# Optimization experiments

Measured on AMD Instinct MI355X. Metric: run time of the kernel, lower is better.

## Reference

```python
import jax, jax.numpy as jnp
import numpy as np

N_NODES = 100000
N_EDGES = 3200000
D_FEAT = 512
HIDDEN = 16
N_CLASSES = 7


def _gcn_conv(x, W, b, src, dst, n_nodes):
    """PyG GCNConv (add_self_loops=True, normalize=True):
    out = D^{-1/2} (A + I) D^{-1/2} X W + b, aggregated at target nodes (dst).
    src/dst already include self loops."""
    h = x @ W  # [N, out_dim] -- transform before scatter (small message dim)
    ones = jnp.ones(dst.shape[0], dtype=x.dtype)
    deg = jax.ops.segment_sum(ones, dst, num_segments=n_nodes)  # in-degree incl. self loop
    dinv = jnp.where(deg > 0, jax.lax.rsqrt(deg), 0.0)
    norm = dinv[src] * dinv[dst]  # [E_tot]
    msg = h[src] * norm[:, None]  # gather + scale
    out = jax.ops.segment_sum(msg, dst, num_segments=n_nodes)  # scatter-add
    return out + b


def setup_inputs() -> dict:
    key = jax.random.key(0)
    k1, k2, k3, k4 = jax.random.split(key, 4)
    x = jax.random.normal(k1, (N_NODES, D_FEAT), dtype=jnp.float32)
    edge_index = jax.random.randint(k2, (2, N_EDGES), 0, N_NODES, dtype=jnp.int64)
    # Glorot-ish init for weights
    W1 = jax.random.normal(k3, (D_FEAT, HIDDEN), dtype=jnp.float32) / np.sqrt(D_FEAT)
    b1 = jnp.zeros((HIDDEN,), dtype=jnp.float32)
    W2 = jax.random.normal(k4, (HIDDEN, N_CLASSES), dtype=jnp.float32) / np.sqrt(HIDDEN)
    b2 = jnp.zeros((N_CLASSES,), dtype=jnp.float32)
    return {"x": x, "edge_index": edge_index, "W1": W1, "b1": b1, "W2": W2, "b2": b2}


def reference(x, edge_index, W1, b1, W2, b2):
    n = x.shape[0]
    loop = jnp.arange(n, dtype=edge_index.dtype)
    src = jnp.concatenate([edge_index[0], loop])  # add self loops (fixed shape)
    dst = jnp.concatenate([edge_index[1], loop])
    h = _gcn_conv(x, W1, b1, src, dst, n)
    h = jax.nn.relu(h)
    # F.dropout(training=self.training): identity in eval/inference baseline
    h = _gcn_conv(h, W2, b2, src, dst, n)
    return jax.nn.log_softmax(h, axis=1)
```

## Files before the change

### kernel.cpp

```cpp
#include <hip/hip_runtime.h>

#define NN 100000
#define NE 3200000
#define DF 512
#define HID 16
#define NC 7
#define NBK 782
#define BCAP 6144
#define SC_B 640
#define SEDG 5000
#define GB 391

__global__ void k_zero_i(int* __restrict__ p, int n) {
    int i = blockIdx.x * blockDim.x + threadIdx.x;
    if (i < n) p[i] = 0;
}

struct SMemScat {
    int stage[SEDG];
    int off[NBK + 1];
    int part[256];
    int cur[NBK];
    int gofs[NBK];
};

__global__ __launch_bounds__(256) void k_fused(const float* __restrict__ x,
                                               const float* __restrict__ W1,
                                               const int* __restrict__ src,
                                               const int* __restrict__ dst,
                                               float* __restrict__ h1,
                                               int* __restrict__ bcnt,
                                               int* __restrict__ pk) {
    __shared__ SMemScat u;
    int tid = threadIdx.x;
    if (blockIdx.x < SC_B) {
        int* stage = u.stage;
        int* off   = u.off;
        int* part  = u.part;
        int* cur   = u.cur;
        int* gofs  = u.gofs;
        int e0 = blockIdx.x * SEDG;
        for (int i = tid; i < NBK; i += 256) cur[i] = 0;
        __syncthreads();
        for (int e = e0 + tid; e < e0 + SEDG; e += 256) atomicAdd(&cur[dst[e] >> 7], 1);
        __syncthreads();
        {
            int base = tid * 4;
            int sum = 0;
#pragma unroll
            for (int j = 0; j < 4; ++j) if (base + j < NBK) sum += cur[base + j];
            part[tid] = sum;
            __syncthreads();
            for (int s2 = 1; s2 < 256; s2 <<= 1) {
                int v = (tid >= s2) ? part[tid - s2] : 0;
                __syncthreads();
                part[tid] += v;
                __syncthreads();
            }
            int run = (tid > 0) ? part[tid - 1] : 0;
#pragma unroll
            for (int j = 0; j < 4; ++j) {
                int idx = base + j;
                if (idx < NBK) { off[idx] = run; run += cur[idx]; }
            }
            if (tid == 0) off[NBK] = SEDG;
        }
        __syncthreads();
        for (int i = tid; i < NBK; i += 256) {
            int h = cur[i];
            int g = h ? atomicAdd(&bcnt[i], h) : 0;
            gofs[i] = g - off[i];
            cur[i] = off[i];
        }
        __syncthreads();
        for (int e = e0 + tid; e < e0 + SEDG; e += 256) {
            int d = dst[e];
            int pos = atomicAdd(&cur[d >> 7], 1);
            stage[pos] = src[e] | ((d & 127) << 17);
        }
        __syncthreads();
        for (int i = tid; i < SEDG; i += 256) {
            int lo = 0, hi = NBK;
            while (hi - lo > 1) { int mid = (lo + hi) >> 1; if (off[mid] <= i) lo = mid; else hi = mid; }
            int idx = gofs[lo] + i;
            if (idx < BCAP) pk[(size_t)lo * BCAP + idx] = stage[i];
        }
        return;
    }
    int gwave = (blockIdx.x - SC_B) * 4 + (tid >> 6);
    int lane = tid & 63;
    long row = (long)gwave * 64 + lane;
    long crow = row < NN ? row : NN - 1;
    const float4* xr = (const float4*)(x + crow * DF);
    float acc[16];
#pragma unroll
    for (int c2 = 0; c2 < 16; ++c2) acc[c2] = 0.f;
#pragma unroll 2
    for (int c = 0; c < 128; ++c) {
        float4 xv = xr[c];
#pragma unroll
        for (int j = 0; j < 4; ++j) {
            float xs = (j == 0) ? xv.x : (j == 1) ? xv.y : (j == 2) ? xv.z : xv.w;
            int k = c * 4 + j;
#pragma unroll
            for (int col = 0; col < 16; ++col)
                acc[col] = fmaf(xs, W1[k * HID + col], acc[col]);
        }
    }
    if (row < NN) {
        float* hp = h1 + row * HID;
#pragma unroll
        for (int q = 0; q < 4; ++q) {
            float4 o;
            o.x = acc[q * 4 + 0]; o.y = acc[q * 4 + 1];
            o.z = acc[q * 4 + 2]; o.w = acc[q * 4 + 3];
            *(float4*)(hp + q * 4) = o;
        }
    }
}

__global__ __launch_bounds__(256) void k_sortB(const int* __restrict__ bcnt,
                                               int* __restrict__ pk,
                                               float* __restrict__ dinv,
                                               float* __restrict__ h1,
                                               int* __restrict__ ptrg,
                                               int* __restrict__ cntg) {
    __shared__ int sorted[BCAP];
    __shared__ int hist[128];
    __shared__ int off[128];
    __shared__ int cur[128];
    __shared__ float dl[128];
    int b = blockIdx.x, tid = threadIdx.x;
    if (tid < 128) hist[tid] = 0;
    __syncthreads();
    int n = min(bcnt[b], BCAP);
    int* p = pk + (size_t)b * BCAP;
    for (int i = tid; i < n; i += 256) atomicAdd(&hist[p[i] >> 17], 1);
    __syncthreads();
    if (tid < 128) off[tid] = hist[tid];
    __syncthreads();
    for (int s2 = 1; s2 < 128; s2 <<= 1) {
        int u = 0;
        if (tid < 128 && tid >= s2) u = off[tid - s2];
        __syncthreads();
        if (tid < 128) off[tid] += u;
        __syncthreads();
    }
    if (tid < 128) {
        int start = off[tid] - hist[tid];
        cur[tid] = start;
        int node = b * 128 + tid;
        float di = rsqrtf((float)hist[tid] + 1.0f);
        dl[tid] = di;
        if (node < NN) {
            dinv[node] = di;
            ptrg[node] = b * BCAP + start;
            cntg[node] = hist[tid];
        }
    }
    __syncthreads();
    for (int i = tid; i < n; i += 256) {
        int v = p[i];
        int pos = atomicAdd(&cur[v >> 17], 1);
        sorted[pos] = v & 0x1FFFF;
    }
    __syncthreads();
    for (int i = tid; i < n; i += 256) p[i] = sorted[i];
    float4* hp = (float4*)(h1 + (size_t)b * 128 * HID);
    for (int i = tid; i < 512; i += 256) {
        int ln = i >> 2;
        int node = b * 128 + ln;
        if (node < NN) {
            float di = dl[ln];
            float4 v = hp[i];
            v.x *= di; v.y *= di; v.z *= di; v.w *= di;
            hp[i] = v;
        }
    }
}

__global__ __launch_bounds__(256) void k_agg1(const int* __restrict__ ptrg,
                                              const int* __restrict__ cntg,
                                              const int* __restrict__ csr,
                                              const float* __restrict__ dinv,
                                              const float* __restrict__ h1s,
                                              const float* __restrict__ b1,
                                              const float* __restrict__ W2,
                                              float* __restrict__ h2s) {
    int tid = threadIdx.x;
    int ch = tid & 15;
    int d = blockIdx.x * 16 + (tid >> 4);
    if (d >= NN) return;
    int st = ptrg[d], n = cntg[d];
    float did = dinv[d];
    float a0 = 0.f, a1 = 0.f;
    int e = st, end = st + n;
    for (; e + 1 < end; e += 2) {
        int s0 = csr[e], s1 = csr[e + 1];
        a0 += h1s[(size_t)s0 * HID + ch];
        a1 += h1s[(size_t)s1 * HID + ch];
    }
    if (e < end) a0 += h1s[(size_t)csr[e] * HID + ch];
    float acc = (a0 + a1 + h1s[(size_t)d * HID + ch]) * did + b1[ch];
    float hr = fmaxf(acc, 0.f);
    float hj = 0.f;
#pragma unroll
    for (int k = 0; k < HID; ++k) {
        float hk = __shfl(hr, k, 16);
        if (ch < NC) hj = fmaf(hk, W2[k * NC + ch], hj);
    }
    if (ch < NC) h2s[(size_t)d * NC + ch] = hj * did;
}

__global__ __launch_bounds__(256) void k_agg2(const int* __restrict__ ptrg,
                                              const int* __restrict__ cntg,
                                              const int* __restrict__ csr,
                                              const float* __restrict__ dinv,
                                              const float* __restrict__ h2s,
                                              const float* __restrict__ b2,
                                              float* __restrict__ out) {
    int tid = threadIdx.x;
    int ch = tid & 7;
    int d = blockIdx.x * 32 + (tid >> 3);
    if (d >= NN) return;
    int st = ptrg[d], n = cntg[d];
    float did = dinv[d];
    float a0 = 0.f, a1 = 0.f;
    int e = st, end = st + n;
    for (; e + 1 < end; e += 2) {
        int s0 = csr[e], s1 = csr[e + 1];
        if (ch < NC) {
            a0 += h2s[(size_t)s0 * NC + ch];
            a1 += h2s[(size_t)s1 * NC + ch];
        }
    }
    if (e < end && ch < NC) a0 += h2s[(size_t)csr[e] * NC + ch];
    float o = -1e30f;
    if (ch < NC) o = (a0 + a1 + h2s[(size_t)d * NC + ch]) * did + b2[ch];
    float m = o;
#pragma unroll
    for (int offm = 1; offm < 8; offm <<= 1) m = fmaxf(m, __shfl_xor(m, offm, 8));
    float ex = (ch < NC) ? expf(o - m) : 0.f;
    float s8 = ex;
#pragma unroll
    for (int offm = 1; offm < 8; offm <<= 1) s8 += __shfl_xor(s8, offm, 8);
    if (ch < NC) out[(size_t)d * NC + ch] = o - m - logf(s8);
}

extern "C" void kernel_launch(void* const* d_in, const int* in_sizes, int n_in,
                              void* d_out, int out_size, void* d_ws, size_t ws_size,
                              hipStream_t stream) {
    const float* x  = (const float*)d_in[0];
    const int*   ei = (const int*)d_in[1];
    const float* W1 = (const float*)d_in[2];
    const float* b1 = (const float*)d_in[3];
    const float* W2 = (const float*)d_in[4];
    const float* b2 = (const float*)d_in[5];
    float* out = (float*)d_out;

    const int* src = ei;
    const int* dst = ei + NE;

    int*   bcnt = (int*)d_ws;
    int*   pk   = bcnt + 784;
    float* dinv = (float*)(pk + (size_t)NBK * BCAP);
    float* h1   = dinv + NN;
    float* h2   = h1 + (size_t)HID * NN;
    int*   ptrg = (int*)(h2 + (size_t)NC * NN);
    int*   cntg = ptrg + NN;

    k_zero_i<<<4, 256, 0, stream>>>(bcnt, 784);
    k_fused <<<SC_B + GB, 256, 0, stream>>>(x, W1, src, dst, h1, bcnt, pk);
    k_sortB <<<NBK, 256, 0, stream>>>(bcnt, pk, dinv, h1, ptrg, cntg);
    k_agg1  <<<(NN + 15) / 16, 256, 0, stream>>>(ptrg, cntg, pk, dinv, h1, b1, W2, h2);
    k_agg2  <<<(NN + 31) / 32, 256, 0, stream>>>(ptrg, cntg, pk, dinv, h2, b2, out);
}
```

Baseline: 214.1 us.

## Replace global bucket atomics with per-block segments and re-sort inside aggregation kernels

```diff
diff --git a/kernel.cpp b/kernel.cpp
--- a/kernel.cpp
+++ b/kernel.cpp
@@ -9,37 +9,24 @@
 #define BCAP 6144
 #define SC_B 640
 #define SEDG 5000
-#define GB 391
-
-__global__ void k_zero_i(int* __restrict__ p, int n) {
-    int i = blockIdx.x * blockDim.x + threadIdx.x;
-    if (i < n) p[i] = 0;
-}
-
-struct SMemScat {
-    int stage[SEDG];
-    int off[NBK + 1];
-    int part[256];
-    int cur[NBK];
-    int gofs[NBK];
-};
+#define OFW 784
+#define GB 782
 
 __global__ __launch_bounds__(256) void k_fused(const float* __restrict__ x,
                                                const float* __restrict__ W1,
                                                const int* __restrict__ src,
                                                const int* __restrict__ dst,
-                                               float* __restrict__ h1,
-                                               int* __restrict__ bcnt,
-                                               int* __restrict__ pk) {
-    __shared__ SMemScat u;
+                                               float* __restrict__ h1p,
+                                               int* __restrict__ seg,
+                                               int* __restrict__ offg) {
+    __shared__ int stage[SEDG];
+    __shared__ int off[NBK + 1];
+    __shared__ int part[256];
+    __shared__ int cur[NBK];
     int tid = threadIdx.x;
     if (blockIdx.x < SC_B) {
-        int* stage = u.stage;
-        int* off   = u.off;
-        int* part  = u.part;
-        int* cur   = u.cur;
-        int* gofs  = u.gofs;
-        int e0 = blockIdx.x * SEDG;
+        int blk = blockIdx.x;
+        int e0 = blk * SEDG;
         for (int i = tid; i < NBK; i += 256) cur[i] = 0;
         __syncthreads();
         for (int e = e0 + tid; e < e0 + SEDG; e += 256) atomicAdd(&cur[dst[e] >> 7], 1);
@@ -66,12 +53,7 @@
             if (tid == 0) off[NBK] = SEDG;
         }
         __syncthreads();
-        for (int i = tid; i < NBK; i += 256) {
-            int h = cur[i];
-            int g = h ? atomicAdd(&bcnt[i], h) : 0;
-            gofs[i] = g - off[i];
-            cur[i] = off[i];
-        }
+        for (int i = tid; i < NBK; i += 256) cur[i] = off[i];
         __syncthreads();
         for (int e = e0 + tid; e < e0 + SEDG; e += 256) {
             int d = dst[e];
@@ -79,24 +61,24 @@
             stage[pos] = src[e] | ((d & 127) << 17);
         }
         __syncthreads();
-        for (int i = tid; i < SEDG; i += 256) {
-            int lo = 0, hi = NBK;
-            while (hi - lo > 1) { int mid = (lo + hi) >> 1; if (off[mid] <= i) lo = mid; else hi = mid; }
-            int idx = gofs[lo] + i;
-            if (idx < BCAP) pk[(size_t)lo * BCAP + idx] = stage[i];
-        }
+        int* sp = seg + (size_t)blk * SEDG;
+        for (int i = tid; i < SEDG; i += 256) sp[i] = stage[i];
+        int* op = offg + (size_t)blk * OFW;
+        for (int i = tid; i <= NBK; i += 256) op[i] = off[i];
         return;
     }
-    int gwave = (blockIdx.x - SC_B) * 4 + (tid >> 6);
+    int w = (blockIdx.x - SC_B) * 4 + (tid >> 6);
+    int g = w >> 1, ks = w & 1;
     int lane = tid & 63;
-    long row = (long)gwave * 64 + lane;
+    long row = (long)g * 64 + lane;
     long crow = row < NN ? row : NN - 1;
-    const float4* xr = (const float4*)(x + crow * DF);
+    const float4* xr = (const float4*)(x + crow * DF + ks * 256);
+    const float* Wk = W1 + ks * 256 * HID;
     float acc[16];
 #pragma unroll
-    for (int c2 = 0; c2 < 16; ++c2) acc[c2] = 0.f;
+    for (int i = 0; i < 16; ++i) acc[i] = 0.f;
 #pragma unroll 2
-    for (int c = 0; c < 128; ++c) {
+    for (int c = 0; c < 64; ++c) {
         float4 xv = xr[c];
 #pragma unroll
         for (int j = 0; j < 4; ++j) {
@@ -104,11 +86,11 @@
             int k = c * 4 + j;
 #pragma unroll
             for (int col = 0; col < 16; ++col)
-                acc[col] = fmaf(xs, W1[k * HID + col], acc[col]);
+                acc[col] = fmaf(xs, Wk[k * HID + col], acc[col]);
         }
     }
     if (row < NN) {
-        float* hp = h1 + row * HID;
+        float* hp = h1p + (size_t)ks * NN * HID + row * HID;
 #pragma unroll
         for (int q = 0; q < 4; ++q) {
             float4 o;
@@ -119,132 +101,208 @@
     }
 }
 
-__global__ __launch_bounds__(256) void k_sortB(const int* __restrict__ bcnt,
-                                               int* __restrict__ pk,
-                                               float* __restrict__ dinv,
-                                               float* __restrict__ h1,
-                                               int* __restrict__ ptrg,
-                                               int* __restrict__ cntg) {
-    __shared__ int sorted[BCAP];
+__global__ __launch_bounds__(256) void k_deg(const int* __restrict__ seg,
+                                             const int* __restrict__ offg,
+                                             float* __restrict__ h1p) {
     __shared__ int hist[128];
-    __shared__ int off[128];
-    __shared__ int cur[128];
     __shared__ float dl[128];
     int b = blockIdx.x, tid = threadIdx.x;
     if (tid < 128) hist[tid] = 0;
     __syncthreads();
-    int n = min(bcnt[b], BCAP);
-    int* p = pk + (size_t)b * BCAP;
-    for (int i = tid; i < n; i += 256) atomicAdd(&hist[p[i] >> 17], 1);
-    __syncthreads();
-    if (tid < 128) off[tid] = hist[tid];
-    __syncthreads();
-    for (int s2 = 1; s2 < 128; s2 <<= 1) {
-        int u = 0;
-        if (tid < 128 && tid >= s2) u = off[tid - s2];
-        __syncthreads();
-        if (tid < 128) off[tid] += u;
-        __syncthreads();
-    }
-    if (tid < 128) {
-        int start = off[tid] - hist[tid];
-        cur[tid] = start;
-        int node = b * 128 + tid;
-        float di = rsqrtf((float)hist[tid] + 1.0f);
-        dl[tid] = di;
-        if (node < NN) {
-            dinv[node] = di;
-            ptrg[node] = b * BCAP + start;
-            cntg[node] = hist[tid];
-        }
-    }
-    __syncthreads();
-    for (int i = tid; i < n; i += 256) {
-        int v = p[i];
-        int pos = atomicAdd(&cur[v >> 17], 1);
-        sorted[pos] = v & 0x1FFFF;
-    }
-    __syncthreads();
-    for (int i = tid; i < n; i += 256) p[i] = sorted[i];
-    float4* hp = (float4*)(h1 + (size_t)b * 128 * HID);
+    for (int r3 = 0; r3 < 3; ++r3) {
+        int sblk = r3 * 256 + tid;
+        if (sblk < SC_B) {
+            int st = offg[(size_t)sblk * OFW + b];
+            int en = offg[(size_t)sblk * OFW + b + 1];
+            const int* sp = seg + (size_t)sblk * SEDG;
+            for (int j = st; j < en; ++j) atomicAdd(&hist[sp[j] >> 17], 1);
+        }
+    }
+    __syncthreads();
+    if (tid < 128) dl[tid] = rsqrtf((float)hist[tid] + 1.0f);
+    __syncthreads();
+    const float4* p1 = (const float4*)(h1p + (size_t)NN * HID);
+    float4* p0 = (float4*)h1p;
     for (int i = tid; i < 512; i += 256) {
         int ln = i >> 2;
         int node = b * 128 + ln;
         if (node < NN) {
             float di = dl[ln];
-            float4 v = hp[i];
-            v.x *= di; v.y *= di; v.z *= di; v.w *= di;
-            hp[i] = v;
-        }
-    }
-}
-
-__global__ __launch_bounds__(256) void k_agg1(const int* __restrict__ ptrg,
-                                              const int* __restrict__ cntg,
-                                              const int* __restrict__ csr,
-                                              const float* __restrict__ dinv,
+            float4 a = p0[(size_t)node * 4 + (i & 3)];
+            float4 c = p1[(size_t)node * 4 + (i & 3)];
+            a.x = (a.x + c.x) * di; a.y = (a.y + c.y) * di;
+            a.z = (a.z + c.z) * di; a.w = (a.w + c.w) * di;
+            p0[(size_t)node * 4 + (i & 3)] = a;
+        }
+    }
+}
+
+__global__ __launch_bounds__(256) void k_agg1(const int* __restrict__ seg,
+                                              const int* __restrict__ offg,
                                               const float* __restrict__ h1s,
                                               const float* __restrict__ b1,
                                               const float* __restrict__ W2,
                                               float* __restrict__ h2s) {
-    int tid = threadIdx.x;
-    int ch = tid & 15;
-    int d = blockIdx.x * 16 + (tid >> 4);
-    if (d >= NN) return;
-    int st = ptrg[d], n = cntg[d];
-    float did = dinv[d];
-    float a0 = 0.f, a1 = 0.f;
-    int e = st, end = st + n;
-    for (; e + 1 < end; e += 2) {
-        int s0 = csr[e], s1 = csr[e + 1];
-        a0 += h1s[(size_t)s0 * HID + ch];
-        a1 += h1s[(size_t)s1 * HID + ch];
-    }
-    if (e < end) a0 += h1s[(size_t)csr[e] * HID + ch];
-    float acc = (a0 + a1 + h1s[(size_t)d * HID + ch]) * did + b1[ch];
-    float hr = fmaxf(acc, 0.f);
-    float hj = 0.f;
-#pragma unroll
-    for (int k = 0; k < HID; ++k) {
-        float hk = __shfl(hr, k, 16);
-        if (ch < NC) hj = fmaf(hk, W2[k * NC + ch], hj);
-    }
-    if (ch < NC) h2s[(size_t)d * NC + ch] = hj * did;
-}
-
-__global__ __launch_bounds__(256) void k_agg2(const int* __restrict__ ptrg,
-                                              const int* __restrict__ cntg,
-                                              const int* __restrict__ csr,
-                                              const float* __restrict__ dinv,
+    __shared__ int sorted[BCAP];
+    __shared__ int hist[128];
+    __shared__ int off2[128];
+    __shared__ int cur2[128];
+    __shared__ float dl[128];
+    int b = blockIdx.x, tid = threadIdx.x;
+    if (tid < 128) hist[tid] = 0;
+    __syncthreads();
+    for (int r3 = 0; r3 < 3; ++r3) {
+        int sblk = r3 * 256 + tid;
+        if (sblk < SC_B) {
+            int st = offg[(size_t)sblk * OFW + b];
+            int en = offg[(size_t)sblk * OFW + b + 1];
+            const int* sp = seg + (size_t)sblk * SEDG;
+            for (int j = st; j < en; ++j) atomicAdd(&hist[sp[j] >> 17], 1);
+        }
+    }
+    __syncthreads();
+    if (tid < 128) off2[tid] = hist[tid];
+    __syncthreads();
+    for (int s2 = 1; s2 < 128; s2 <<= 1) {
+        int u = 0;
+        if (tid < 128 && tid >= s2) u = off2[tid - s2];
+        __syncthreads();
+        if (tid < 128) off2[tid] += u;
+        __syncthreads();
+    }
+    if (tid < 128) {
+        int start = off2[tid] - hist[tid];
+        off2[tid] = start;
+        cur2[tid] = start;
+        dl[tid] = rsqrtf((float)hist[tid] + 1.0f);
+    }
+    __syncthreads();
+    for (int r3 = 0; r3 < 3; ++r3) {
+        int sblk = r3 * 256 + tid;
+        if (sblk < SC_B) {
+            int st = offg[(size_t)sblk * OFW + b];
+            int en = offg[(size_t)sblk * OFW + b + 1];
+            const int* sp = seg + (size_t)sblk * SEDG;
+            for (int j = st; j < en; ++j) {
+                int v = sp[j];
+                int pos = atomicAdd(&cur2[v >> 17], 1);
+                if (pos < BCAP) sorted[pos] = v & 0x1FFFF;
+            }
+        }
+    }
+    __syncthreads();
+    int ch = tid & 15, g2 = tid >> 4;
+    for (int it = 0; it < 8; ++it) {
+        int ln = it * 16 + g2;
+        int node = b * 128 + ln;
+        int st = off2[ln];
+        int end = min(st + hist[ln], BCAP);
+        float a0 = 0.f, a1 = 0.f;
+        int e = st;
+        for (; e + 1 < end; e += 2) {
+            int s0 = sorted[e], s1 = sorted[e + 1];
+            a0 += h1s[(size_t)s0 * HID + ch];
+            a1 += h1s[(size_t)s1 * HID + ch];
+        }
+        if (e < end) a0 += h1s[(size_t)sorted[e] * HID + ch];
+        if (node < NN) {
+            float did = dl[ln];
+            float acc = (a0 + a1 + h1s[(size_t)node * HID + ch]) * did + b1[ch];
+            float hr = fmaxf(acc, 0.f);
+            float hj = 0.f;
+#pragma unroll
+            for (int k = 0; k < HID; ++k) {
+                float hk = __shfl(hr, k, 16);
+                if (ch < NC) hj = fmaf(hk, W2[k * NC + ch], hj);
+            }
+            if (ch < NC) h2s[(size_t)node * NC + ch] = hj * did;
+        } else {
+#pragma unroll
+            for (int k = 0; k < HID; ++k) (void)__shfl(0.f, k, 16);
+        }
+    }
+}
+
+__global__ __launch_bounds__(256) void k_agg2(const int* __restrict__ seg,
+                                              const int* __restrict__ offg,
                                               const float* __restrict__ h2s,
                                               const float* __restrict__ b2,
                                               float* __restrict__ out) {
-    int tid = threadIdx.x;
-    int ch = tid & 7;
-    int d = blockIdx.x * 32 + (tid >> 3);
-    if (d >= NN) return;
-    int st = ptrg[d], n = cntg[d];
-    float did = dinv[d];
-    float a0 = 0.f, a1 = 0.f;
-    int e = st, end = st + n;
-    for (; e + 1 < end; e += 2) {
-        int s0 = csr[e], s1 = csr[e + 1];
-        if (ch < NC) {
-            a0 += h2s[(size_t)s0 * NC + ch];
-            a1 += h2s[(size_t)s1 * NC + ch];
-        }
-    }
-    if (e < end && ch < NC) a0 += h2s[(size_t)csr[e] * NC + ch];
-    float o = -1e30f;
-    if (ch < NC) o = (a0 + a1 + h2s[(size_t)d * NC + ch]) * did + b2[ch];
-    float m = o;
-#pragma unroll
-    for (int offm = 1; offm < 8; offm <<= 1) m = fmaxf(m, __shfl_xor(m, offm, 8));
-    float ex = (ch < NC) ? expf(o - m) : 0.f;
-    float s8 = ex;
-#pragma unroll
-    for (int offm = 1; offm < 8; offm <<= 1) s8 += __shfl_xor(s8, offm, 8);
-    if (ch < NC) out[(size_t)d * NC + ch] = o - m - logf(s8);
+    __shared__ int sorted[BCAP];
+    __shared__ int hist[128];
+    __shared__ int off2[128];
+    __shared__ int cur2[128];
+    __shared__ float dl[128];
+    int b = blockIdx.x, tid = threadIdx.x;
+    if (tid < 128) hist[tid] = 0;
+    __syncthreads();
+    for (int r3 = 0; r3 < 3; ++r3) {
+        int sblk = r3 * 256 + tid;
+        if (sblk < SC_B) {
+            int st = offg[(size_t)sblk * OFW + b];
+            int en = offg[(size_t)sblk * OFW + b + 1];
+            const int* sp = seg + (size_t)sblk * SEDG;
+            for (int j = st; j < en; ++j) atomicAdd(&hist[sp[j] >> 17], 1);
+        }
+    }
+    __syncthreads();
+    if (tid < 128) off2[tid] = hist[tid];
+    __syncthreads();
+    for (int s2 = 1; s2 < 128; s2 <<= 1) {
+        int u = 0;
+        if (tid < 128 && tid >= s2) u = off2[tid - s2];
+        __syncthreads();
+        if (tid < 128) off2[tid] += u;
+        __syncthreads();
+    }
+    if (tid < 128) {
+        int start = off2[tid] - hist[tid];
+        off2[tid] = start;
+        cur2[tid] = start;
+        dl[tid] = rsqrtf((float)hist[tid] + 1.0f);
+    }
+    __syncthreads();
+    for (int r3 = 0; r3 < 3; ++r3) {
+        int sblk = r3 * 256 + tid;
+        if (sblk < SC_B) {
+            int st = offg[(size_t)sblk * OFW + b];
+            int en = offg[(size_t)sblk * OFW + b + 1];
+            const int* sp = seg + (size_t)sblk * SEDG;
+            for (int j = st; j < en; ++j) {
+                int v = sp[j];
+                int pos = atomicAdd(&cur2[v >> 17], 1);
+                if (pos < BCAP) sorted[pos] = v & 0x1FFFF;
+            }
+        }
+    }
+    __syncthreads();
+    int ch = tid & 7, g2 = tid >> 3;
+    for (int it = 0; it < 4; ++it) {
+        int ln = it * 32 + g2;
+        int node = b * 128 + ln;
+        int st = off2[ln];
+        int end = min(st + hist[ln], BCAP);
+        float a0 = 0.f, a1 = 0.f;
+        int e = st;
+        for (; e + 1 < end; e += 2) {
+            int s0 = sorted[e], s1 = sorted[e + 1];
+            if (ch < NC) {
+                a0 += h2s[(size_t)s0 * NC + ch];
+                a1 += h2s[(size_t)s1 * NC + ch];
+            }
+        }
+        if (e < end && ch < NC) a0 += h2s[(size_t)sorted[e] * NC + ch];
+        float o = -1e30f;
+        if (ch < NC) o = (a0 + a1 + h2s[(size_t)node * NC + ch]) * dl[ln] + b2[ch];
+        float m = o;
+#pragma unroll
+        for (int offm = 1; offm < 8; offm <<= 1) m = fmaxf(m, __shfl_xor(m, offm, 8));
+        float ex = (ch < NC) ? expf(o - m) : 0.f;
+        float s8 = ex;
+#pragma unroll
+        for (int offm = 1; offm < 8; offm <<= 1) s8 += __shfl_xor(s8, offm, 8);
+        if (node < NN && ch < NC) out[(size_t)node * NC + ch] = o - m - logf(s8);
+    }
 }
 
 extern "C" void kernel_launch(void* const* d_in, const int* in_sizes, int n_in,
@@ -261,17 +319,13 @@
     const int* src = ei;
     const int* dst = ei + NE;
 
-    int*   bcnt = (int*)d_ws;
-    int*   pk   = bcnt + 784;
-    float* dinv = (float*)(pk + (size_t)NBK * BCAP);
-    float* h1   = dinv + NN;
-    float* h2   = h1 + (size_t)HID * NN;
-    int*   ptrg = (int*)(h2 + (size_t)NC * NN);
-    int*   cntg = ptrg + NN;
-
-    k_zero_i<<<4, 256, 0, stream>>>(bcnt, 784);
-    k_fused <<<SC_B + GB, 256, 0, stream>>>(x, W1, src, dst, h1, bcnt, pk);
-    k_sortB <<<NBK, 256, 0, stream>>>(bcnt, pk, dinv, h1, ptrg, cntg);
-    k_agg1  <<<(NN + 15) / 16, 256, 0, stream>>>(ptrg, cntg, pk, dinv, h1, b1, W2, h2);
-    k_agg2  <<<(NN + 31) / 32, 256, 0, stream>>>(ptrg, cntg, pk, dinv, h2, b2, out);
-}
+    int*   seg  = (int*)d_ws;
+    int*   offg = seg + (size_t)SC_B * SEDG;
+    float* h1p  = (float*)(offg + (size_t)SC_B * OFW);
+    float* h2   = h1p + (size_t)2 * NN * HID;
+
+    k_fused <<<SC_B + GB, 256, 0, stream>>>(x, W1, src, dst, h1p, seg, offg);
+    k_deg   <<<NBK, 256, 0, stream>>>(seg, offg, h1p);
+    k_agg1  <<<NBK, 256, 0, stream>>>(seg, offg, h1p, b1, W2, h2);
+    k_agg2  <<<NBK, 256, 0, stream>>>(seg, offg, h2, b2, out);
+}
```

New measurement: 439.6 us. 2.05x slower.
